# Kernel tuning notes

Measured on AMD Instinct MI355X. Metric: run time of the kernel, lower is better.

The kernel has to match this reference:

```python
import jax, jax.numpy as jnp
import numpy as np

N_NODES = 100000
N_FEAT = 256
OUT_DIM = 128
NNZ_X = 1_600_000
NNZ_A = 1_600_000
DROPOUT = 0.0  # layer default; floor(1-p+u) mask is all-ones -> deterministic


def setup_inputs() -> dict:
    key = jax.random.key(0)
    k = jax.random.split(key, 7)
    feat_rows = jax.random.randint(k[0], (NNZ_X,), 0, N_NODES, dtype=jnp.int32)
    feat_cols = jax.random.randint(k[1], (NNZ_X,), 0, N_FEAT, dtype=jnp.int32)
    feat_vals = jax.random.normal(k[2], (NNZ_X,), dtype=jnp.float32)
    adj_rows = jax.random.randint(k[3], (NNZ_A,), 0, N_NODES, dtype=jnp.int32)
    adj_cols = jax.random.randint(k[4], (NNZ_A,), 0, N_NODES, dtype=jnp.int32)
    adj_vals = jax.random.uniform(k[5], (NNZ_A,), dtype=jnp.float32)
    glorot_std = np.sqrt(2.0 / (N_FEAT + OUT_DIM)).astype(np.float32)
    W = jax.random.normal(k[6], (N_FEAT, OUT_DIM), dtype=jnp.float32) * glorot_std
    return {
        "feat_rows": feat_rows, "feat_cols": feat_cols, "feat_vals": feat_vals,
        "adj_rows": adj_rows, "adj_cols": adj_cols, "adj_vals": adj_vals,
        "W": W, "n_nodes": N_NODES,
    }


def reference(feat_rows, feat_cols, feat_vals, adj_rows, adj_cols, adj_vals, W, n_nodes):
    # sparse dropout on feature nonzeros: mask = floor((1-p) + uniform) in {0,1}
    u = jax.random.uniform(jax.random.key(1), feat_vals.shape, dtype=feat_vals.dtype)
    keep = jnp.floor((1.0 - DROPOUT) + u)
    vals = feat_vals * keep * (1.0 / (1.0 - DROPOUT))
    # X @ W : gather W rows by feature column, scale by nnz value, scatter-add into node rows
    xw = jax.ops.segment_sum(vals[:, None] * W[feat_cols], feat_rows,
                             num_segments=n_nodes)  # [N, D]
    # A @ (X @ W) : gather node rows by edge source, scale by edge weight, scatter-add to dest
    agg = jax.ops.segment_sum(adj_vals[:, None] * xw[adj_cols], adj_rows,
                              num_segments=n_nodes)  # [N, D]
    return jax.nn.relu(agg)
```

## Files before the change

### kernel.cpp

```cpp
#include <hip/hip_runtime.h>
#include <hip/hip_fp16.h>

#define OUT_DIM 128
#define NPS 256
#define NS_MAX 400
#define CAP_S 4608
#define SBLK1 256
#define EPT1 16
#define CHUNK1 (SBLK1 * EPT1)
#define SBLK2 256
#define GBLK 256

__global__ __launch_bounds__(SBLK1) void scatter1_kernel(
    const int* __restrict__ adj_rows, const int* __restrict__ adj_cols,
    const float* __restrict__ adj_vals, int nnz_a, int nCkA,
    const int* __restrict__ feat_rows, const int* __restrict__ feat_cols,
    const float* __restrict__ feat_vals, int nnz_x,
    int* __restrict__ cur, int2* __restrict__ pay, int ns)
{
    __shared__ int2 s_stage[CHUNK1];
    __shared__ unsigned short s_bin[CHUNK1];
    __shared__ int s_hist[NS_MAX];
    __shared__ int s_excl[NS_MAX];
    __shared__ int s_gbase[NS_MAX];

    int tid = threadIdx.x;
    bool isA = ((int)blockIdx.x < nCkA);
    const int* rows; const int* cols; const float* vals;
    int nnz, start, matbase;
    if (isA) {
        rows = adj_rows; cols = adj_cols; vals = adj_vals; nnz = nnz_a;
        start = (int)blockIdx.x * CHUNK1; matbase = 0;
    } else {
        rows = feat_rows; cols = feat_cols; vals = feat_vals; nnz = nnz_x;
        start = ((int)blockIdx.x - nCkA) * CHUNK1; matbase = ns;
    }
    int total = nnz - start; if (total > CHUNK1) total = CHUNK1;

    for (int i = tid; i < ns; i += SBLK1) s_hist[i] = 0;
    __syncthreads();

    int rr[EPT1]; int cc[EPT1]; float vv[EPT1];
    #pragma unroll
    for (int k = 0; k < EPT1; ++k) {
        int e = start + k * SBLK1 + tid;
        rr[k] = -1;
        if (e < nnz) {
            rr[k] = rows[e]; cc[k] = cols[e]; vv[k] = vals[e];
            atomicAdd(&s_hist[rr[k] >> 8], 1);
        }
    }
    __syncthreads();

    if (tid < 64) {
        int carry = 0;
        for (int seg = 0; seg < ns; seg += 64) {
            int idx = seg + tid;
            int x = (idx < ns) ? s_hist[idx] : 0;
            int incl = x;
            #pragma unroll
            for (int off = 1; off < 64; off <<= 1) {
                int y = __shfl_up(incl, off, 64);
                if (tid >= off) incl += y;
            }
            if (idx < ns) s_excl[idx] = carry + incl - x;
            carry += __shfl(incl, 63, 64);
        }
    }
    __syncthreads();

    for (int i = tid; i < ns; i += SBLK1) {
        int c = s_hist[i];
        s_gbase[i] = (c > 0) ? atomicAdd(&cur[matbase + i], c) : 0;
        s_hist[i] = 0;
    }
    __syncthreads();

    #pragma unroll
    for (int k = 0; k < EPT1; ++k) {
        if (rr[k] >= 0) {
            int b = rr[k] >> 8;
            int rl = rr[k] & 255;
            int pos = s_excl[b] + atomicAdd(&s_hist[b], 1);
            s_stage[pos] = make_int2((rl << 17) | cc[k], __float_as_int(vv[k]));
            s_bin[pos] = (unsigned short)b;
        }
    }
    __syncthreads();

    for (int i = tid; i < total; i += SBLK1) {
        int b = s_bin[i];
        int g = s_gbase[b] + (i - s_excl[b]);
        if (g < CAP_S)
            pay[(size_t)(matbase + b) * CAP_S + g] = s_stage[i];
    }
}

__global__ __launch_bounds__(SBLK2) void sort2_kernel(
    const int* __restrict__ cur, int2* __restrict__ pay,
    int2* __restrict__ row_span, int ns, int n_nodes)
{
    __shared__ int2 sedge[CAP_S];
    __shared__ int s_cnt[NPS];
    int b = blockIdx.x;
    int tid = threadIdx.x;
    int count = cur[b]; if (count > CAP_S) count = CAP_S;
    int2* region = pay + (size_t)b * CAP_S;

    s_cnt[tid] = 0;
    __syncthreads();
    for (int i = tid; i < count; i += SBLK2) {
        int2 e = region[i];
        sedge[i] = e;
        atomicAdd(&s_cnt[((unsigned)e.x) >> 17], 1);
    }
    __syncthreads();
    int v = s_cnt[tid];
    for (int off = 1; off < NPS; off <<= 1) {
        int t = (tid >= off) ? s_cnt[tid - off] : 0;
        __syncthreads();
        s_cnt[tid] += t;
        __syncthreads();
    }
    int excl = s_cnt[tid] - v;
    int m = (b >= ns) ? 1 : 0;
    int g = (b - m * ns) * NPS + tid;
    if (g < n_nodes)
        row_span[(size_t)m * n_nodes + g] = make_int2(b * CAP_S + excl, v);
    __syncthreads();
    s_cnt[tid] = excl;
    __syncthreads();
    for (int i = tid; i < count; i += SBLK2) {
        int2 e = sedge[i];
        int rl = ((unsigned)e.x) >> 17;
        int pos = atomicAdd(&s_cnt[rl], 1);
        region[pos] = make_int2(e.x & 0x1FFFF, e.y);
    }
}

__global__ void wcast_kernel(const float* __restrict__ W, __half* __restrict__ W16, int n) {
    int i = blockIdx.x * blockDim.x + threadIdx.x;
    if (i < n) W16[i] = __float2half(W[i]);
}

__global__ __launch_bounds__(GBLK) void gather_xw_kernel(
    const int2* __restrict__ row_span, const int2* __restrict__ pay,
    const __half* __restrict__ W16, __half* __restrict__ XW, int n_nodes)
{
    int tid = threadIdx.x;
    int lane = tid & 15;
    int node = blockIdx.x * 16 + (tid >> 4);
    if (node >= n_nodes) return;
    int2 span = row_span[(size_t)n_nodes + node];
    int s = span.x, cnt = span.y;
    const int4* Wv = (const int4*)W16;
    float a0=0,a1=0,a2=0,a3=0,a4=0,a5=0,a6=0,a7=0;
    for (int base = 0; base < cnt; base += 16) {
        int mm = cnt - base; if (mm > 16) mm = 16;
        int2 pl = make_int2(0, 0);
        if (lane < mm) pl = pay[s + base + lane];
        #pragma unroll 4
        for (int j = 0; j < mm; ++j) {
            int c = __shfl(pl.x, j, 16);
            float v = __int_as_float(__shfl(pl.y, j, 16));
            union { int4 i4; __half2 h[4]; } u;
            u.i4 = Wv[(size_t)c * 16 + lane];
            float2 f0 = __half22float2(u.h[0]);
            float2 f1 = __half22float2(u.h[1]);
            float2 f2 = __half22float2(u.h[2]);
            float2 f3 = __half22float2(u.h[3]);
            a0 += v * f0.x; a1 += v * f0.y; a2 += v * f1.x; a3 += v * f1.y;
            a4 += v * f2.x; a5 += v * f2.y; a6 += v * f3.x; a7 += v * f3.y;
        }
    }
    union { int4 i4; __half2 h[4]; } o;
    o.h[0] = __floats2half2_rn(a0, a1);
    o.h[1] = __floats2half2_rn(a2, a3);
    o.h[2] = __floats2half2_rn(a4, a5);
    o.h[3] = __floats2half2_rn(a6, a7);
    ((int4*)(XW + (size_t)node * OUT_DIM))[lane] = o.i4;
}

__global__ __launch_bounds__(GBLK) void gather_agg_kernel(
    const int2* __restrict__ row_span, const int2* __restrict__ pay,
    const __half* __restrict__ XW, float* __restrict__ out, int n_nodes)
{
    int tid = threadIdx.x;
    int lane = tid & 15;
    int node = blockIdx.x * 16 + (tid >> 4);
    if (node >= n_nodes) return;
    int2 span = row_span[node];
    int s = span.x, cnt = span.y;
    const int4* Xv = (const int4*)XW;
    float a0=0,a1=0,a2=0,a3=0,a4=0,a5=0,a6=0,a7=0;
    for (int base = 0; base < cnt; base += 16) {
        int mm = cnt - base; if (mm > 16) mm = 16;
        int2 pl = make_int2(0, 0);
        if (lane < mm) pl = pay[s + base + lane];
        #pragma unroll 4
        for (int j = 0; j < mm; ++j) {
            int c = __shfl(pl.x, j, 16);
            float v = __int_as_float(__shfl(pl.y, j, 16));
            union { int4 i4; __half2 h[4]; } u;
            u.i4 = Xv[(size_t)c * 16 + lane];
            float2 f0 = __half22float2(u.h[0]);
            float2 f1 = __half22float2(u.h[1]);
            float2 f2 = __half22float2(u.h[2]);
            float2 f3 = __half22float2(u.h[3]);
            a0 += v * f0.x; a1 += v * f0.y; a2 += v * f1.x; a3 += v * f1.y;
            a4 += v * f2.x; a5 += v * f2.y; a6 += v * f3.x; a7 += v * f3.y;
        }
    }
    float4 lo, hi;
    lo.x = fmaxf(a0, 0.f); lo.y = fmaxf(a1, 0.f);
    lo.z = fmaxf(a2, 0.f); lo.w = fmaxf(a3, 0.f);
    hi.x = fmaxf(a4, 0.f); hi.y = fmaxf(a5, 0.f);
    hi.z = fmaxf(a6, 0.f); hi.w = fmaxf(a7, 0.f);
    float4* orow = (float4*)(out + (size_t)node * OUT_DIM);
    orow[2 * lane]     = lo;
    orow[2 * lane + 1] = hi;
}

extern "C" void kernel_launch(void* const* d_in, const int* in_sizes, int n_in,
                              void* d_out, int out_size, void* d_ws, size_t ws_size,
                              hipStream_t stream) {
    const int*   feat_rows = (const int*)d_in[0];
    const int*   feat_cols = (const int*)d_in[1];
    const float* feat_vals = (const float*)d_in[2];
    const int*   adj_rows  = (const int*)d_in[3];
    const int*   adj_cols  = (const int*)d_in[4];
    const float* adj_vals  = (const float*)d_in[5];
    const float* W         = (const float*)d_in[6];
    float*       out       = (float*)d_out;

    const int nnz_x   = in_sizes[0];
    const int nnz_a   = in_sizes[3];
    const int n_w     = in_sizes[6];
    const int n_nodes = out_size / OUT_DIM;
    const int ns      = (n_nodes + NPS - 1) / NPS;

    char* p = (char*)d_ws;
    __half* XW   = (__half*)p;  p += (size_t)n_nodes * OUT_DIM * sizeof(__half);
    __half* W16  = (__half*)p;  p += (size_t)n_w * sizeof(__half);
    p = (char*)(((uintptr_t)p + 15) & ~(uintptr_t)15);
    int2* pay    = (int2*)p;    p += (size_t)2 * ns * CAP_S * sizeof(int2);
    int2* row_span = (int2*)p;  p += (size_t)2 * n_nodes * sizeof(int2);
    int* cur     = (int*)p;     p += (size_t)2 * ns * sizeof(int);

    hipMemsetAsync(cur, 0, (size_t)2 * ns * sizeof(int), stream);

    wcast_kernel<<<(n_w + 255) / 256, 256, 0, stream>>>(W, W16, n_w);

    const int nCkA = (nnz_a + CHUNK1 - 1) / CHUNK1;
    const int nCkX = (nnz_x + CHUNK1 - 1) / CHUNK1;
    scatter1_kernel<<<nCkA + nCkX, SBLK1, 0, stream>>>(
        adj_rows, adj_cols, adj_vals, nnz_a, nCkA,
        feat_rows, feat_cols, feat_vals, nnz_x,
        cur, pay, ns);

    sort2_kernel<<<2 * ns, SBLK2, 0, stream>>>(cur, pay, row_span, ns, n_nodes);

    const int gnb = (n_nodes + 15) / 16;
    gather_xw_kernel<<<gnb, GBLK, 0, stream>>>(row_span, pay, W16, XW, n_nodes);
    gather_agg_kernel<<<gnb, GBLK, 0, stream>>>(row_span, pay, XW, out, n_nodes);
}
```

Baseline: 255.8 us.

## Build CSR with global count/scan/atomic placement and fuse A placement into XW gather

```diff
diff --git a/kernel.cpp b/kernel.cpp
--- a/kernel.cpp
+++ b/kernel.cpp
@@ -2,154 +2,114 @@
 #include <hip/hip_fp16.h>
 
 #define OUT_DIM 128
-#define NPS 256
-#define NS_MAX 400
-#define CAP_S 4608
-#define SBLK1 256
-#define EPT1 16
-#define CHUNK1 (SBLK1 * EPT1)
-#define SBLK2 256
 #define GBLK 256
-
-__global__ __launch_bounds__(SBLK1) void scatter1_kernel(
-    const int* __restrict__ adj_rows, const int* __restrict__ adj_cols,
-    const float* __restrict__ adj_vals, int nnz_a, int nCkA,
-    const int* __restrict__ feat_rows, const int* __restrict__ feat_cols,
-    const float* __restrict__ feat_vals, int nnz_x,
-    int* __restrict__ cur, int2* __restrict__ pay, int ns)
-{
-    __shared__ int2 s_stage[CHUNK1];
-    __shared__ unsigned short s_bin[CHUNK1];
-    __shared__ int s_hist[NS_MAX];
-    __shared__ int s_excl[NS_MAX];
-    __shared__ int s_gbase[NS_MAX];
-
-    int tid = threadIdx.x;
-    bool isA = ((int)blockIdx.x < nCkA);
-    const int* rows; const int* cols; const float* vals;
-    int nnz, start, matbase;
-    if (isA) {
-        rows = adj_rows; cols = adj_cols; vals = adj_vals; nnz = nnz_a;
-        start = (int)blockIdx.x * CHUNK1; matbase = 0;
-    } else {
-        rows = feat_rows; cols = feat_cols; vals = feat_vals; nnz = nnz_x;
-        start = ((int)blockIdx.x - nCkA) * CHUNK1; matbase = ns;
-    }
-    int total = nnz - start; if (total > CHUNK1) total = CHUNK1;
-
-    for (int i = tid; i < ns; i += SBLK1) s_hist[i] = 0;
-    __syncthreads();
-
-    int rr[EPT1]; int cc[EPT1]; float vv[EPT1];
-    #pragma unroll
-    for (int k = 0; k < EPT1; ++k) {
-        int e = start + k * SBLK1 + tid;
-        rr[k] = -1;
-        if (e < nnz) {
-            rr[k] = rows[e]; cc[k] = cols[e]; vv[k] = vals[e];
-            atomicAdd(&s_hist[rr[k] >> 8], 1);
-        }
-    }
-    __syncthreads();
-
-    if (tid < 64) {
-        int carry = 0;
-        for (int seg = 0; seg < ns; seg += 64) {
-            int idx = seg + tid;
-            int x = (idx < ns) ? s_hist[idx] : 0;
-            int incl = x;
-            #pragma unroll
-            for (int off = 1; off < 64; off <<= 1) {
-                int y = __shfl_up(incl, off, 64);
-                if (tid >= off) incl += y;
-            }
-            if (idx < ns) s_excl[idx] = carry + incl - x;
-            carry += __shfl(incl, 63, 64);
-        }
-    }
-    __syncthreads();
-
-    for (int i = tid; i < ns; i += SBLK1) {
-        int c = s_hist[i];
-        s_gbase[i] = (c > 0) ? atomicAdd(&cur[matbase + i], c) : 0;
-        s_hist[i] = 0;
-    }
-    __syncthreads();
-
-    #pragma unroll
-    for (int k = 0; k < EPT1; ++k) {
-        if (rr[k] >= 0) {
-            int b = rr[k] >> 8;
-            int rl = rr[k] & 255;
-            int pos = s_excl[b] + atomicAdd(&s_hist[b], 1);
-            s_stage[pos] = make_int2((rl << 17) | cc[k], __float_as_int(vv[k]));
-            s_bin[pos] = (unsigned short)b;
-        }
-    }
-    __syncthreads();
-
-    for (int i = tid; i < total; i += SBLK1) {
-        int b = s_bin[i];
-        int g = s_gbase[b] + (i - s_excl[b]);
-        if (g < CAP_S)
-            pay[(size_t)(matbase + b) * CAP_S + g] = s_stage[i];
-    }
-}
-
-__global__ __launch_bounds__(SBLK2) void sort2_kernel(
-    const int* __restrict__ cur, int2* __restrict__ pay,
-    int2* __restrict__ row_span, int ns, int n_nodes)
-{
-    __shared__ int2 sedge[CAP_S];
-    __shared__ int s_cnt[NPS];
-    int b = blockIdx.x;
-    int tid = threadIdx.x;
-    int count = cur[b]; if (count > CAP_S) count = CAP_S;
-    int2* region = pay + (size_t)b * CAP_S;
-
-    s_cnt[tid] = 0;
-    __syncthreads();
-    for (int i = tid; i < count; i += SBLK2) {
-        int2 e = region[i];
-        sedge[i] = e;
-        atomicAdd(&s_cnt[((unsigned)e.x) >> 17], 1);
-    }
-    __syncthreads();
-    int v = s_cnt[tid];
-    for (int off = 1; off < NPS; off <<= 1) {
-        int t = (tid >= off) ? s_cnt[tid - off] : 0;
-        __syncthreads();
-        s_cnt[tid] += t;
-        __syncthreads();
-    }
-    int excl = s_cnt[tid] - v;
-    int m = (b >= ns) ? 1 : 0;
-    int g = (b - m * ns) * NPS + tid;
-    if (g < n_nodes)
-        row_span[(size_t)m * n_nodes + g] = make_int2(b * CAP_S + excl, v);
-    __syncthreads();
-    s_cnt[tid] = excl;
-    __syncthreads();
-    for (int i = tid; i < count; i += SBLK2) {
-        int2 e = sedge[i];
-        int rl = ((unsigned)e.x) >> 17;
-        int pos = atomicAdd(&s_cnt[rl], 1);
-        region[pos] = make_int2(e.x & 0x1FFFF, e.y);
-    }
-}
+#define SCAN_TPB 256
+#define SCAN_TILE 1024
+
 
 __global__ void wcast_kernel(const float* __restrict__ W, __half* __restrict__ W16, int n) {
     int i = blockIdx.x * blockDim.x + threadIdx.x;
     if (i < n) W16[i] = __float2half(W[i]);
 }
 
-__global__ __launch_bounds__(GBLK) void gather_xw_kernel(
-    const int2* __restrict__ row_span, const int2* __restrict__ pay,
+__global__ __launch_bounds__(256) void count_kernel(
+    const int* __restrict__ adj_rows, int nnz_a,
+    const int* __restrict__ feat_rows, int nnz_x,
+    int* __restrict__ cnt, int n_nodes)
+{
+    int i = blockIdx.x * 256 + threadIdx.x;
+    if (i < nnz_a)
+        atomicAdd(&cnt[adj_rows[i]], 1);
+    else if (i < nnz_a + nnz_x)
+        atomicAdd(&cnt[n_nodes + feat_rows[i - nnz_a]], 1);
+}
+
+__global__ __launch_bounds__(SCAN_TPB) void scan1_kernel(
+    const int* __restrict__ cnt, int* __restrict__ cursor,
+    int* __restrict__ blockSums, int N2)
+{
+    __shared__ int sd[SCAN_TPB];
+    int tid = threadIdx.x;
+    int base = blockIdx.x * SCAN_TILE + tid * 4;
+    int v0 = (base + 0 < N2) ? cnt[base + 0] : 0;
+    int v1 = (base + 1 < N2) ? cnt[base + 1] : 0;
+    int v2 = (base + 2 < N2) ? cnt[base + 2] : 0;
+    int v3 = (base + 3 < N2) ? cnt[base + 3] : 0;
+    int ts = v0 + v1 + v2 + v3;
+    sd[tid] = ts;
+    __syncthreads();
+    for (int off = 1; off < SCAN_TPB; off <<= 1) {
+        int t = (tid >= off) ? sd[tid - off] : 0;
+        __syncthreads();
+        sd[tid] += t;
+        __syncthreads();
+    }
+    int excl = sd[tid] - ts;
+    if (base + 0 < N2) cursor[base + 0] = excl;
+    if (base + 1 < N2) cursor[base + 1] = excl + v0;
+    if (base + 2 < N2) cursor[base + 2] = excl + v0 + v1;
+    if (base + 3 < N2) cursor[base + 3] = excl + v0 + v1 + v2;
+    if (tid == SCAN_TPB - 1) blockSums[blockIdx.x] = sd[tid];
+}
+
+__global__ __launch_bounds__(SCAN_TPB) void scan2_kernel(int* __restrict__ blockSums, int nblk)
+{
+    __shared__ int sd[SCAN_TPB];
+    int tid = threadIdx.x;
+    int v = (tid < nblk) ? blockSums[tid] : 0;
+    sd[tid] = v;
+    __syncthreads();
+    for (int off = 1; off < SCAN_TPB; off <<= 1) {
+        int t = (tid >= off) ? sd[tid - off] : 0;
+        __syncthreads();
+        sd[tid] += t;
+        __syncthreads();
+    }
+    if (tid < nblk) blockSums[tid] = sd[tid] - v;
+}
+
+__global__ __launch_bounds__(256) void scan3_kernel(
+    const int* __restrict__ cnt, int* __restrict__ cursor,
+    const int* __restrict__ blockSums, int2* __restrict__ row_span, int N2)
+{
+    int i = blockIdx.x * 256 + threadIdx.x;
+    if (i < N2) {
+        int b = cursor[i] + blockSums[i >> 10];
+        cursor[i] = b;
+        row_span[i] = make_int2(b, cnt[i]);
+    }
+}
+
+__global__ __launch_bounds__(256) void place_x_kernel(
+    const int* __restrict__ rows, const int* __restrict__ cols,
+    const float* __restrict__ vals, int nnz,
+    int* __restrict__ cursor, int2* __restrict__ pay, int n_nodes)
+{
+    int i = blockIdx.x * 256 + threadIdx.x;
+    if (i < nnz) {
+        int pos = atomicAdd(&cursor[n_nodes + rows[i]], 1);
+        pay[pos] = make_int2(cols[i], __float_as_int(vals[i]));
+    }
+}
+
+__global__ __launch_bounds__(GBLK) void placeA_xw_kernel(
+    const int* __restrict__ rows, const int* __restrict__ cols,
+    const float* __restrict__ vals, int nnz_a, int nbA,
+    int* __restrict__ cursor,
+    const int2* __restrict__ row_span, int2* __restrict__ pay,
     const __half* __restrict__ W16, __half* __restrict__ XW, int n_nodes)
 {
     int tid = threadIdx.x;
+    if ((int)blockIdx.x < nbA) {
+        int i = (int)blockIdx.x * 256 + tid;
+        if (i < nnz_a) {
+            int pos = atomicAdd(&cursor[rows[i]], 1);
+            pay[pos] = make_int2(cols[i], __float_as_int(vals[i]));
+        }
+        return;
+    }
     int lane = tid & 15;
-    int node = blockIdx.x * 16 + (tid >> 4);
+    int node = ((int)blockIdx.x - nbA) * 16 + (tid >> 4);
     if (node >= n_nodes) return;
     int2 span = row_span[(size_t)n_nodes + node];
     int s = span.x, cnt = span.y;
@@ -181,7 +141,7 @@
     ((int4*)(XW + (size_t)node * OUT_DIM))[lane] = o.i4;
 }
 
-__global__ __launch_bounds__(GBLK) void gather_agg_kernel(
+__global__ __launch_bounds__(GBLK, 4) void gather_agg_kernel(
     const int2* __restrict__ row_span, const int2* __restrict__ pay,
     const __half* __restrict__ XW, float* __restrict__ out, int n_nodes)
 {
@@ -193,16 +153,22 @@
     int s = span.x, cnt = span.y;
     const int4* Xv = (const int4*)XW;
     float a0=0,a1=0,a2=0,a3=0,a4=0,a5=0,a6=0,a7=0;
+    int2 pl = make_int2(0, 0);
+    if (lane < cnt) pl = pay[s + lane];
     for (int base = 0; base < cnt; base += 16) {
-        int mm = cnt - base; if (mm > 16) mm = 16;
-        int2 pl = make_int2(0, 0);
-        if (lane < mm) pl = pay[s + base + lane];
-        #pragma unroll 4
-        for (int j = 0; j < mm; ++j) {
+        int4 w[16];
+        #pragma unroll
+        for (int j = 0; j < 16; ++j) {
             int c = __shfl(pl.x, j, 16);
+            w[j] = Xv[(size_t)((c << 4) | lane)];
+        }
+        int2 pln = make_int2(0, 0);
+        if (base + 16 + lane < cnt) pln = pay[s + base + 16 + lane];
+        #pragma unroll
+        for (int j = 0; j < 16; ++j) {
             float v = __int_as_float(__shfl(pl.y, j, 16));
             union { int4 i4; __half2 h[4]; } u;
-            u.i4 = Xv[(size_t)c * 16 + lane];
+            u.i4 = w[j];
             float2 f0 = __half22float2(u.h[0]);
             float2 f1 = __half22float2(u.h[1]);
             float2 f2 = __half22float2(u.h[2]);
@@ -210,6 +176,7 @@
             a0 += v * f0.x; a1 += v * f0.y; a2 += v * f1.x; a3 += v * f1.y;
             a4 += v * f2.x; a5 += v * f2.y; a6 += v * f3.x; a7 += v * f3.y;
         }
+        pl = pln;
     }
     float4 lo, hi;
     lo.x = fmaxf(a0, 0.f); lo.y = fmaxf(a1, 0.f);
@@ -237,30 +204,40 @@
     const int nnz_a   = in_sizes[3];
     const int n_w     = in_sizes[6];
     const int n_nodes = out_size / OUT_DIM;
-    const int ns      = (n_nodes + NPS - 1) / NPS;
+    const int N2      = 2 * n_nodes;
 
     char* p = (char*)d_ws;
     __half* XW   = (__half*)p;  p += (size_t)n_nodes * OUT_DIM * sizeof(__half);
     __half* W16  = (__half*)p;  p += (size_t)n_w * sizeof(__half);
     p = (char*)(((uintptr_t)p + 15) & ~(uintptr_t)15);
-    int2* pay    = (int2*)p;    p += (size_t)2 * ns * CAP_S * sizeof(int2);
-    int2* row_span = (int2*)p;  p += (size_t)2 * n_nodes * sizeof(int2);
-    int* cur     = (int*)p;     p += (size_t)2 * ns * sizeof(int);
-
-    hipMemsetAsync(cur, 0, (size_t)2 * ns * sizeof(int), stream);
+    int2* pay    = (int2*)p;    p += (size_t)(nnz_a + nnz_x) * sizeof(int2);
+    int2* row_span = (int2*)p;  p += (size_t)N2 * sizeof(int2);
+    int* cnt     = (int*)p;     p += (size_t)N2 * sizeof(int);
+    int* cursor  = (int*)p;     p += (size_t)N2 * sizeof(int);
+    int* blockSums = (int*)p;   p += 256 * sizeof(int);
+
+    (void)hipMemsetAsync(cnt, 0, (size_t)N2 * sizeof(int), stream);
 
     wcast_kernel<<<(n_w + 255) / 256, 256, 0, stream>>>(W, W16, n_w);
 
-    const int nCkA = (nnz_a + CHUNK1 - 1) / CHUNK1;
-    const int nCkX = (nnz_x + CHUNK1 - 1) / CHUNK1;
-    scatter1_kernel<<<nCkA + nCkX, SBLK1, 0, stream>>>(
-        adj_rows, adj_cols, adj_vals, nnz_a, nCkA,
-        feat_rows, feat_cols, feat_vals, nnz_x,
-        cur, pay, ns);
-
-    sort2_kernel<<<2 * ns, SBLK2, 0, stream>>>(cur, pay, row_span, ns, n_nodes);
-
+    const int tot = nnz_a + nnz_x;
+    count_kernel<<<(tot + 255) / 256, 256, 0, stream>>>(
+        adj_rows, nnz_a, feat_rows, nnz_x, cnt, n_nodes);
+
+    const int nblk1 = (N2 + SCAN_TILE - 1) / SCAN_TILE;
+    scan1_kernel<<<nblk1, SCAN_TPB, 0, stream>>>(cnt, cursor, blockSums, N2);
+    scan2_kernel<<<1, SCAN_TPB, 0, stream>>>(blockSums, nblk1);
+    scan3_kernel<<<(N2 + 255) / 256, 256, 0, stream>>>(
+        cnt, cursor, blockSums, row_span, N2);
+
+    place_x_kernel<<<(nnz_x + 255) / 256, 256, 0, stream>>>(
+        feat_rows, feat_cols, feat_vals, nnz_x, cursor, pay, n_nodes);
+
+    const int nbA = (nnz_a + 255) / 256;
     const int gnb = (n_nodes + 15) / 16;
-    gather_xw_kernel<<<gnb, GBLK, 0, stream>>>(row_span, pay, W16, XW, n_nodes);
+    placeA_xw_kernel<<<nbA + gnb, GBLK, 0, stream>>>(
+        adj_rows, adj_cols, adj_vals, nnz_a, nbA,
+        cursor, row_span, pay, W16, XW, n_nodes);
+
     gather_agg_kernel<<<gnb, GBLK, 0, stream>>>(row_span, pay, XW, out, n_nodes);
 }
```

New measurement: 530.7 us. 107% more time.
